# Kernel optimization log

Measured on AMD Instinct MI355X. Metric: run time of the kernel, lower is better.

## Reference

```python
import jax, jax.numpy as jnp
from jax import lax
import numpy as np

DIM = 384; NH = 8; N = 16; K = 4; DIN = 768; DTR = 24  # d_model, heads, d_state, d_conv, d_inner, dt_rank
B = 8; Hh = 48; Ww = 48


def _ln(x, g, b):
    m = jnp.mean(x, -1, keepdims=True)
    v = jnp.mean((x - m) ** 2, -1, keepdims=True)
    return (x - m) / jnp.sqrt(v + 1e-5) * g + b


def _mamba(x, in_w, in_b, conv_w, conv_b, xp_w, dt_w, dt_b, A_log, Dp, out_w, out_b):
    # x: (B, L, DIM)
    Bb, L, _ = x.shape
    xz = x @ in_w.T + in_b                      # (B, L, 2*DIN)
    xm, z = xz[..., :DIN], xz[..., DIN:]
    # depthwise causal conv over sequence
    xc = jnp.pad(xm.transpose(0, 2, 1), ((0, 0), (0, 0), (K - 1, 0)))  # (B, DIN, L+K-1)
    xconv = lax.conv_general_dilated(xc, conv_w[:, None, :], (1,), 'VALID',
                                     feature_group_count=DIN,
                                     dimension_numbers=('NCH', 'OIH', 'NCH'))
    u = jax.nn.silu((xconv + conv_b[None, :, None]).transpose(0, 2, 1))  # (B, L, DIN)
    dbc = u @ xp_w.T                            # (B, L, DTR + 2N)
    delta = jax.nn.softplus(dbc[..., :DTR] @ dt_w.T + dt_b)  # (B, L, DIN)
    Bm = dbc[..., DTR:DTR + N]                  # (B, L, N)
    Cm = dbc[..., DTR + N:]                     # (B, L, N)
    A = -jnp.exp(A_log)                         # (DIN, N)

    def step(h, inp):
        d_t, B_t, C_t, u_t = inp                # (B,DIN),(B,N),(B,N),(B,DIN)
        dA = jnp.exp(d_t[:, :, None] * A)       # (B, DIN, N)
        h = h * dA + d_t[:, :, None] * B_t[:, None, :] * u_t[:, :, None]
        y = jnp.einsum('bdn,bn->bd', h, C_t)
        return h, y

    h0 = jnp.zeros((Bb, DIN, N), x.dtype)
    xs = (delta.transpose(1, 0, 2), Bm.transpose(1, 0, 2), Cm.transpose(1, 0, 2), u.transpose(1, 0, 2))
    _, ys = lax.scan(step, h0, xs)
    y = ys.transpose(1, 0, 2) + u * Dp
    y = y * jax.nn.silu(z)
    return y @ out_w.T + out_b


def _forward(x, n1_g, n1_b, ap_w, ap_b, n2_g, n2_b, in_w, in_b, conv_w, conv_b, xp_w, dt_w, dt_b,
             A_log, Dp, out_w, out_b, mod_w1, mod_b1, mod_w2, mod_b2, n3_g, n3_b,
             fc1_w, fc1_b, fc2_w, fc2_b):
    Bb, C, Hc, Wc = x.shape
    xs = x.reshape(Bb, C, Hc * Wc).transpose(0, 2, 1)          # (B, L, C)
    xn = _ln(xs, n1_g, n1_b)
    attn = jax.nn.softmax(xn @ ap_w.T + ap_b, axis=1)          # softmax over sequence
    gc = jnp.einsum('bln,blc->bnc', attn, xn).mean(1)          # (B, C)
    mod = jax.nn.silu(gc @ mod_w1.T + mod_b1) @ mod_w2.T + mod_b2
    xn2 = _ln(xs, n2_g, n2_b)
    mo = _mamba(xn2, in_w, in_b, conv_w, conv_b, xp_w, dt_w, dt_b, A_log, Dp, out_w, out_b)
    mo = mo * (1.0 + mod[:, None, :])
    xs = xs + mo
    h = _ln(xs, n3_g, n3_b)
    h = jax.nn.gelu(h @ fc1_w.T + fc1_b) @ fc2_w.T + fc2_b
    xs = xs + h
    return xs.transpose(0, 2, 1).reshape(Bb, C, Hc, Wc)


def setup_inputs() -> dict:
    key = jax.random.key(0)
    ks = jax.random.split(key, 16)
    s = 0.02
    p = {}
    p['x'] = jax.random.normal(ks[0], (B, DIM, Hh, Ww), jnp.float32)
    p['n1_g'] = jnp.ones((DIM,), jnp.float32); p['n1_b'] = jnp.zeros((DIM,), jnp.float32)
    p['ap_w'] = jax.random.normal(ks[1], (NH, DIM), jnp.float32) * s; p['ap_b'] = jnp.zeros((NH,), jnp.float32)
    p['n2_g'] = jnp.ones((DIM,), jnp.float32); p['n2_b'] = jnp.zeros((DIM,), jnp.float32)
    p['in_w'] = jax.random.normal(ks[2], (2 * DIN, DIM), jnp.float32) * s; p['in_b'] = jnp.zeros((2 * DIN,), jnp.float32)
    p['conv_w'] = jax.random.normal(ks[3], (DIN, K), jnp.float32) * s; p['conv_b'] = jnp.zeros((DIN,), jnp.float32)
    p['xp_w'] = jax.random.normal(ks[4], (DTR + 2 * N, DIN), jnp.float32) * s
    p['dt_w'] = jax.random.normal(ks[5], (DIN, DTR), jnp.float32) * s
    p['dt_b'] = jax.random.uniform(ks[6], (DIN,), jnp.float32, minval=-4.0, maxval=-2.0)
    p['A_log'] = jnp.log(jnp.tile(jnp.arange(1, N + 1, dtype=jnp.float32), (DIN, 1)))
    p['Dp'] = jnp.ones((DIN,), jnp.float32)
    p['out_w'] = jax.random.normal(ks[7], (DIM, DIN), jnp.float32) * s; p['out_b'] = jnp.zeros((DIM,), jnp.float32)
    p['mod_w1'] = jax.random.normal(ks[8], (2 * DIM, DIM), jnp.float32) * s; p['mod_b1'] = jnp.zeros((2 * DIM,), jnp.float32)
    p['mod_w2'] = jax.random.normal(ks[9], (DIM, 2 * DIM), jnp.float32) * s; p['mod_b2'] = jnp.zeros((DIM,), jnp.float32)
    p['n3_g'] = jnp.ones((DIM,), jnp.float32); p['n3_b'] = jnp.zeros((DIM,), jnp.float32)
    p['fc1_w'] = jax.random.normal(ks[10], (4 * DIM, DIM), jnp.float32) * s; p['fc1_b'] = jnp.zeros((4 * DIM,), jnp.float32)
    p['fc2_w'] = jax.random.normal(ks[11], (DIM, 4 * DIM), jnp.float32) * s; p['fc2_b'] = jnp.zeros((DIM,), jnp.float32)
    return p


def reference(x, n1_g, n1_b, ap_w, ap_b, n2_g, n2_b, in_w, in_b, conv_w, conv_b, xp_w, dt_w, dt_b,
              A_log, Dp, out_w, out_b, mod_w1, mod_b1, mod_w2, mod_b2, n3_g, n3_b,
              fc1_w, fc1_b, fc2_w, fc2_b):
    return _forward(x, n1_g, n1_b, ap_w, ap_b, n2_g, n2_b, in_w, in_b, conv_w, conv_b, xp_w,
                    dt_w, dt_b, A_log, Dp, out_w, out_b, mod_w1, mod_b1, mod_w2, mod_b2,
                    n3_g, n3_b, fc1_w, fc1_b, fc2_w, fc2_b)
```

## Files before the change

kernel.cpp:

```cpp
#include <hip/hip_runtime.h>
#include <math.h>

#define DIMC 384
#define NHD 8
#define NSTATE 16
#define DINN 768
#define DTRK 24
#define BB 8
#define LSEQ 2304
#define MROWS (BB*LSEQ)
#define NCH 64
#define TCH 36
#define L2E 1.44269504f

typedef unsigned short u16;
typedef short bf16x8 __attribute__((ext_vector_type(8)));
typedef float f32x4 __attribute__((ext_vector_type(4)));

__device__ __forceinline__ float sigmoid_(float x){ return 1.f/(1.f+__expf(-x)); }
__device__ __forceinline__ float silu_(float x){ return x*sigmoid_(x); }
__device__ __forceinline__ float softplus_(float x){ return (x>20.f)?x:log1pf(__expf(x)); }
__device__ __forceinline__ float gelu_(float x){
  float x3=x*x*x;
  return 0.5f*x*(1.f+tanhf(0.7978845608028654f*(x+0.044715f*x3)));
}
__device__ __forceinline__ float bfu2f(u16 u){
  union{unsigned int i; float f;} c; c.i=((unsigned int)u)<<16; return c.f;
}
__device__ __forceinline__ u16 f2bfu(float f){
  union{float f; unsigned int i;} c; c.f=f;
  unsigned int r = c.i + 0x7FFFu + ((c.i>>16)&1u);
  return (u16)(r>>16);
}
__device__ __forceinline__ void gl_lds16(const u16* g, u16* l){
  __builtin_amdgcn_global_load_lds((__attribute__((address_space(1))) void*)g,
      (__attribute__((address_space(3))) void*)l, 16, 0, 0);
}

__device__ __forceinline__ u16 swzw(const float* __restrict__ s, int o, int KT,
                                    int Nsrc, int Ksrc){
  int e = o&7, l = (o>>3)&63, rest = o>>9;
  int kt = rest % KT, nt = rest / KT;
  int n = nt*16 + (l&15);
  int k = kt*32 + ((l>>4)<<3) + e;
  return (n<Nsrc && k<Ksrc) ? f2bfu(s[(size_t)n*Ksrc + k]) : (u16)0;
}

#define O1 589824
#define O2 688128
#define O3 983040
#define O4 1572864
#define O5 2162688
#define O6 2187264
#define OEND 2190336
__global__ void k_cvtall(const float* __restrict__ inw, const float* __restrict__ xpw,
    const float* __restrict__ outw, const float* __restrict__ fc1w,
    const float* __restrict__ fc2w, const float* __restrict__ dtw,
    u16* __restrict__ inw_b, u16* __restrict__ xpw_pad, u16* __restrict__ outw_b,
    u16* __restrict__ fc1w_b, u16* __restrict__ fc2w_b, u16* __restrict__ dtw_pad,
    float* __restrict__ gc){
  int i = blockIdx.x*256+threadIdx.x;
  if(i >= OEND) return;
  if(i < O1){ inw_b[i]   = swzw(inw,  i,    12, 1536, 384); }
  else if(i < O2){ xpw_pad[i-O1] = swzw(xpw,  i-O1, 24, 56,   768); }
  else if(i < O3){ outw_b[i-O2]  = swzw(outw, i-O2, 24, 384,  768); }
  else if(i < O4){ fc1w_b[i-O3]  = swzw(fc1w, i-O3, 12, 1536, 384); }
  else if(i < O5){ fc2w_b[i-O4]  = swzw(fc2w, i-O4, 48, 384,  1536); }
  else if(i < O6){ dtw_pad[i-O5] = swzw(dtw,  i-O5, 1,  768,  24); }
  else { gc[i-O6]=0.f; }
}

__global__ void k_transpose(const float* __restrict__ x, float* __restrict__ xs){
  __shared__ float tile[32][33];
  int b = blockIdx.z;
  int t0 = blockIdx.x*32, c0 = blockIdx.y*32;
  int tx = threadIdx.x, ty = threadIdx.y;
  const float* xb = x + (size_t)b*DIMC*LSEQ;
  #pragma unroll
  for(int q=0;q<4;q++)
    tile[ty+q*8][tx] = xb[(size_t)(c0+ty+q*8)*LSEQ + t0+tx];
  __syncthreads();
  float* xsb = xs + (size_t)b*LSEQ*DIMC;
  #pragma unroll
  for(int q=0;q<4;q++)
    xsb[(size_t)(t0+ty+q*8)*DIMC + c0+tx] = tile[tx][ty+q*8];
}

__global__ __launch_bounds__(64) void k_lnstats(const float* __restrict__ xs,
   const float* __restrict__ g1,const float* __restrict__ b1,
   const float* __restrict__ g2,const float* __restrict__ b2,
   const float* __restrict__ apw,const float* __restrict__ apb,
   float* __restrict__ meanr, float* __restrict__ rstdr,
   u16* __restrict__ xn2, float* __restrict__ scores){
  int row = blockIdx.x;
  int lane = threadIdx.x;
  const float* xr = xs + (size_t)row*DIMC;
  float v[6];
  float s=0.f, s2=0.f;
  #pragma unroll
  for(int i=0;i<6;i++){ v[i]=xr[lane+i*64]; s+=v[i]; s2+=v[i]*v[i]; }
  #pragma unroll
  for(int m=32;m>=1;m>>=1){ s += __shfl_xor(s,m); s2 += __shfl_xor(s2,m); }
  float mean = s*(1.f/DIMC);
  float var  = s2*(1.f/DIMC)-mean*mean;
  float rstd = rsqrtf(var+1e-5f);
  if(lane==0){ meanr[row]=mean; rstdr[row]=rstd; }
  float xv1[6];
  #pragma unroll
  for(int i=0;i<6;i++){
    int c = lane+i*64;
    float nx = (v[i]-mean)*rstd;
    xv1[i] = nx*g1[c]+b1[c];
    xn2[(size_t)row*DIMC+c] = f2bfu(nx*g2[c]+b2[c]);
  }
  #pragma unroll
  for(int h=0;h<NHD;h++){
    float p=0.f;
    #pragma unroll
    for(int i=0;i<6;i++) p += xv1[i]*apw[h*DIMC+lane+i*64];
    #pragma unroll
    for(int m=32;m>=1;m>>=1) p += __shfl_xor(p,m);
    if(lane==0) scores[(size_t)row*NHD+h]=p+apb[h];
  }
}

__global__ __launch_bounds__(256) void k_softmax_L(float* __restrict__ sc){
  int bh = blockIdx.x; int b = bh>>3, h = bh&7;
  int tid = threadIdx.x;
  __shared__ float red[8];
  const size_t base = (size_t)b*LSEQ*NHD + h;
  float mx = -1e30f;
  for(int l=tid;l<LSEQ;l+=256) mx = fmaxf(mx, sc[base + (size_t)l*NHD]);
  #pragma unroll
  for(int m=32;m>=1;m>>=1) mx = fmaxf(mx, __shfl_xor(mx,m));
  if((tid&63)==0) red[tid>>6]=mx;
  __syncthreads();
  mx = fmaxf(fmaxf(red[0],red[1]),fmaxf(red[2],red[3]));
  float sum=0.f;
  for(int l=tid;l<LSEQ;l+=256) sum += __expf(sc[base+(size_t)l*NHD]-mx);
  #pragma unroll
  for(int m=32;m>=1;m>>=1) sum += __shfl_xor(sum,m);
  if((tid&63)==0) red[4+(tid>>6)]=sum;
  __syncthreads();
  float inv = 1.f/(red[4]+red[5]+red[6]+red[7]);
  for(int l=tid;l<LSEQ;l+=256){
    size_t idx = base+(size_t)l*NHD;
    sc[idx] = __expf(sc[idx]-mx)*inv;
  }
}

__global__ __launch_bounds__(384) void k_gc(const float* __restrict__ attn,
    const float* __restrict__ xs, const float* __restrict__ meanr,
    const float* __restrict__ rstdr, const float* __restrict__ g1,
    const float* __restrict__ b1, float* __restrict__ gc){
  int b = blockIdx.x; int chunk = blockIdx.y; int c = threadIdx.x;
  int l0 = chunk*48;
  float acc=0.f, accw=0.f;
  for(int l=0;l<48;l++){
    int row = b*LSEQ + l0+l;
    const float* a = attn + (size_t)row*NHD;
    float ww = (((a[0]+a[1])+(a[2]+a[3]))+((a[4]+a[5])+(a[6]+a[7])))*0.125f;
    acc  += ww*(xs[(size_t)row*DIMC+c]-meanr[row])*rstdr[row];
    accw += ww;
  }
  atomicAdd(&gc[b*DIMC+c], acc*g1[c]+accw*b1[c]);
}

__global__ __launch_bounds__(256) void k_mod1(const float* __restrict__ gc,
    const float* __restrict__ w1, const float* __restrict__ b1,
    float* __restrict__ modh){
  int b = blockIdx.x; int n = blockIdx.y*64 + (threadIdx.x>>2);
  int sub = threadIdx.x&3;
  const float4* g = (const float4*)(gc + b*DIMC) + sub*24;
  const float4* wr = (const float4*)(w1 + (size_t)n*DIMC) + sub*24;
  float acc=0.f;
  #pragma unroll
  for(int k=0;k<24;k++){
    float4 a=g[k], w=wr[k];
    acc += a.x*w.x + a.y*w.y + a.z*w.z + a.w*w.w;
  }
  acc += __shfl_xor(acc,1); acc += __shfl_xor(acc,2);
  if(sub==0) modh[b*768+n] = silu_(acc+b1[n]);
}
__global__ __launch_bounds__(256) void k_mod2(const float* __restrict__ modh,
    const float* __restrict__ w2, const float* __restrict__ b2,
    float* __restrict__ mod){
  int b = blockIdx.x; int n = blockIdx.y*64 + (threadIdx.x>>2);
  int sub = threadIdx.x&3;
  const float4* g = (const float4*)(modh + b*768) + sub*48;
  const float4* wr = (const float4*)(w2 + (size_t)n*768) + sub*48;
  float acc=0.f;
  #pragma unroll
  for(int k=0;k<48;k++){
    float4 a=g[k], w=wr[k];
    acc += a.x*w.x + a.y*w.y + a.z*w.z + a.w*w.w;
  }
  acc += __shfl_xor(acc,1); acc += __shfl_xor(acc,2);
  if(sub==0) mod[b*DIMC+n] = acc+b2[n];
}

#define MG_STEP(KT_I, CUR, BIN, BOUT, VMSTR)                                   \
  {                                                                            \
    if((KT_I)+1 < KT){                                                         \
      _Pragma("unroll")                                                        \
      for(int j=0;j<4;j++)                                                     \
        BOUT[j] = *reinterpret_cast<const bf16x8*>(wp + 512 + j*(KT*512));     \
    }                                                                          \
    asm volatile("s_waitcnt " VMSTR ::: "memory");                             \
    __builtin_amdgcn_s_barrier();                                              \
    bf16x8 af[4];                                                              \
    {                                                                          \
      const u16* lbase = &lA[CUR][lofs];                                       \
      _Pragma("unroll")                                                        \
      for(int i=0;i<4;i++)                                                     \
        af[i] = *reinterpret_cast<const bf16x8*>(lbase + i*128);               \
    }                                                                          \
    asm volatile("s_waitcnt lgkmcnt(0)" ::: "memory");                         \
    __builtin_amdgcn_s_barrier();                                              \
    if((KT_I)+2 < KT){                                                         \
      gl_lds16(Ag0 + ((KT_I)+2)*32,      (CUR)? ld1 : ld0);                    \
      gl_lds16(Ag0 + ((KT_I)+2)*32 + 16, (CUR)? hd1 : hd0);                    \
    }                                                                          \
    _Pragma("unroll")                                                          \
    for(int i=0;i<4;i++)                                                       \
      _Pragma("unroll")                                                        \
      for(int j=0;j<4;j++)                                                     \
        acc[i][j] = __builtin_amdgcn_mfma_f32_16x16x32_bf16(af[i], BIN[j],     \
                                                            acc[i][j], 0,0,0);\
    wp += 512;                                                                 \
  }

template<int EPI, int K>
__global__ __launch_bounds__(256,4) void k_mgemm(
    const u16* __restrict__ A, const u16* __restrict__ Wf,
    const float* __restrict__ bias, void* __restrict__ outp,
    int N, const float* __restrict__ aux, void* __restrict__ outp2)
{
  constexpr int KT = K/32;
  __shared__ u16 lA[2][4096];
  int tid = threadIdx.x;
  int m0 = blockIdx.x*128, n0 = blockIdx.y*128;
  int wid = tid>>6, lane = tid&63;
  int wr = wid>>1, wc = wid&1;
  int lrow = lane&15, lk = lane>>4;
  f32x4 acc[4][4];
  #pragma unroll
  for(int i=0;i<4;i++)
    #pragma unroll
    for(int j=0;j<4;j++){ acc[i][j][0]=0.f; acc[i][j][1]=0.f; acc[i][j][2]=0.f; acc[i][j][3]=0.f; }

  int r0 = tid & 127, k0 = tid >> 7;
  const u16* Ag0 = A + (size_t)(m0+r0)*K + k0*8;
  const u16* wp  = Wf + ((size_t)((n0>>4) + wc*4)*KT)*512 + (size_t)lane*8;
  const int lofs = (lk*128 + wr*64 + lrow)*8;
  u16* ld0 = &lA[0][tid*8];  u16* hd0 = &lA[0][2048+tid*8];
  u16* ld1 = &lA[1][tid*8];  u16* hd1 = &lA[1][2048+tid*8];

  gl_lds16(Ag0,    ld0);
  gl_lds16(Ag0+16, hd0);
  if(KT>1){
    gl_lds16(Ag0+32, ld1);
    gl_lds16(Ag0+48, hd1);
  }
  bf16x8 bA[4], bB[4];
  #pragma unroll
  for(int j=0;j<4;j++) bA[j] = *reinterpret_cast<const bf16x8*>(wp + j*(KT*512));

  if(KT==1){
    MG_STEP(0, 0, bA, bB, "vmcnt(0)")
  } else {
    MG_STEP(0, 0, bA, bB, "vmcnt(4)")
    for(int kt=1; kt<KT-1; kt+=2){
      MG_STEP(kt,   1, bB, bA, "vmcnt(6)")
      MG_STEP(kt+1, 0, bA, bB, "vmcnt(6)")
    }
    MG_STEP(KT-1, 1, bB, bA, "vmcnt(0)")
  }

  #pragma unroll
  for(int i=0;i<4;i++){
    int row = m0 + wr*64 + i*16 + lk*4;
    #pragma unroll
    for(int j=0;j<4;j++){
      int col = n0 + wc*64 + j*16 + lrow;
      float bc = bias ? bias[col] : 0.f;
      f32x4 v = acc[i][j];
      if(EPI==0){
        u16* o = (u16*)outp;
        #pragma unroll
        for(int r=0;r<4;r++) o[(size_t)(row+r)*N + col] = f2bfu(v[r]+bc);
      } else if(EPI==1){
        u16* o = (u16*)outp;
        #pragma unroll
        for(int r=0;r<4;r++) o[(size_t)(row+r)*N + col] = f2bfu(gelu_(v[r]+bc));
      } else if(EPI==2){
        float* o = (float*)outp;
        int bi = row/LSEQ;
        float sc = 1.f + aux[bi*DIMC + col];
        #pragma unroll
        for(int r=0;r<4;r++) o[(size_t)(row+r)*DIMC + col] += (v[r]+bc)*sc;
      } else if(EPI==3){
        float* o = (float*)outp;
        int bi = row/LSEQ, t = row - bi*LSEQ;
        float4 s;
        s.x = aux[(size_t)(row+0)*DIMC+col] + v[0] + bc;
        s.y = aux[(size_t)(row+1)*DIMC+col] + v[1] + bc;
        s.z = aux[(size_t)(row+2)*DIMC+col] + v[2] + bc;
        s.w = aux[(size_t)(row+3)*DIMC+col] + v[3] + bc;
        *reinterpret_cast<float4*>(&o[((size_t)(bi*DIMC+col))*LSEQ + t]) = s;
      } else if(EPI==4){
        float* o = (float*)outp;
        if(col < N){
          #pragma unroll
          for(int r=0;r<4;r++) o[(size_t)(row+r)*N + col] = v[r]+bc;
        }
      } else if(EPI==5){
        u16* o = (col < 768) ? (u16*)outp : (u16*)outp2;
        int cc = (col < 768) ? col : col - 768;
        #pragma unroll
        for(int r=0;r<4;r++) o[(size_t)(row+r)*768 + cc] = f2bfu(v[r]+bc);
      } else if(EPI==6){
        float* o = (float*)outp;
        u16* o2 = (u16*)outp2;
        #pragma unroll
        for(int r=0;r<4;r++){
          float val = v[r];
          if(col < 56) o[(size_t)(row+r)*56 + col] = val;
          if(col < 32) o2[(size_t)(row+r)*32 + col] = (col<DTRK)? f2bfu(val) : (u16)0;
        }
      } else {
        u16* o = (u16*)outp;
        #pragma unroll
        for(int r=0;r<4;r++) o[(size_t)(row+r)*N + col] = f2bfu(softplus_(v[r]+bc));
      }
    }
  }
}

__global__ void k_conv(const u16* __restrict__ xm, const float* __restrict__ cw,
                       const float* __restrict__ cb, u16* __restrict__ u){
  int idx = blockIdx.x*256+threadIdx.x;
  if(idx >= MROWS*(DINN/8)) return;
  int j = idx % (DINN/8); int r = idx / (DINN/8);
  int t = r % LSEQ; int d0 = j*8;
  float4 w4_[8];
  #pragma unroll
  for(int e=0;e<8;e++) w4_[e] = reinterpret_cast<const float4*>(cw)[d0+e];
  float acc[8];
  #pragma unroll
  for(int e=0;e<8;e++) acc[e]=cb[d0+e];
  #pragma unroll
  for(int k=0;k<4;k++){
    int tt=t+k-3;
    if(tt>=0){
      uint4 v = *reinterpret_cast<const uint4*>(&xm[(size_t)(r+k-3)*DINN + d0]);
      unsigned vv[4]={v.x,v.y,v.z,v.w};
      #pragma unroll
      for(int e=0;e<8;e++){
        u16 raw = (e&1)? (u16)(vv[e>>1]>>16) : (u16)(vv[e>>1]&0xffffu);
        float wk = (k==0)? w4_[e].x : (k==1)? w4_[e].y : (k==2)? w4_[e].z : w4_[e].w;
        acc[e] += bfu2f(raw)*wk;
      }
    }
  }
  u16 outv[8];
  #pragma unroll
  for(int e=0;e<8;e++) outv[e]=f2bfu(silu_(acc[e]));
  *reinterpret_cast<uint4*>(&u[(size_t)r*DINN+d0]) = *reinterpret_cast<const uint4*>(outv);
}

__global__ __launch_bounds__(256) void k_scan1(
  const u16* __restrict__ dt_, const u16* __restrict__ u_,
  const float* __restrict__ dbc, const float* __restrict__ alog,
  float* __restrict__ ssum, float* __restrict__ hloc)
{
  __shared__ float Bsh[TCH][16];
  int bid = blockIdx.x;
  int b = bid/(NCH*3); int rem = bid%(NCH*3); int ch = rem/3; int dblk = rem%3;
  int tid = threadIdx.x; int d = dblk*256 + tid;
  size_t rbase = (size_t)b*LSEQ + (size_t)ch*TCH;
  for(int j=tid; j<TCH*16; j+=256){
    int row=j>>4, n=j&15;
    Bsh[row][n] = dbc[(rbase+row)*56 + DTRK + n];
  }
  float Acl2[16];
  float a0 = -__expf(alog[(size_t)d*16])*L2E;
  bool fast = true;
  #pragma unroll
  for(int n=0;n<16;n++){
    Acl2[n] = -__expf(alog[(size_t)d*16+n])*L2E;
    float tgt = (float)(n+1)*a0;
    fast = fast && (fabsf(Acl2[n]-tgt) <= 1e-4f*fabsf(tgt));
  }
  float h[16];
  #pragma unroll
  for(int n=0;n<16;n++) h[n]=0.f;
  float S=0.f;
  const u16* dtp = dt_ + rbase*DINN + d;
  const u16* up  = u_  + rbase*DINN + d;
  __syncthreads();
  if(fast){
    for(int t=0;t<TCH;t++){
      float dt = bfu2f(dtp[(size_t)t*DINN]);
      float uv = bfu2f(up[(size_t)t*DINN]);
      float G = dt*uv;
      S += dt;
      float e = exp2f(dt*a0), w = e;
      const float4* b4 = (const float4*)Bsh[t];
      float4 B0=b4[0],B1=b4[1],B2=b4[2],B3=b4[3];
      float Bv[16]={B0.x,B0.y,B0.z,B0.w,B1.x,B1.y,B1.z,B1.w,
                    B2.x,B2.y,B2.z,B2.w,B3.x,B3.y,B3.z,B3.w};
      #pragma unroll
      for(int n=0;n<16;n++){ h[n] = h[n]*w + G*Bv[n]; w *= e; }
    }
  } else {
    for(int t=0;t<TCH;t++){
      float dt = bfu2f(dtp[(size_t)t*DINN]);
      float uv = bfu2f(up[(size_t)t*DINN]);
      float G = dt*uv;
      S += dt;
      const float4* b4 = (const float4*)Bsh[t];
      float4 B0=b4[0],B1=b4[1],B2=b4[2],B3=b4[3];
      float Bv[16]={B0.x,B0.y,B0.z,B0.w,B1.x,B1.y,B1.z,B1.w,
                    B2.x,B2.y,B2.z,B2.w,B3.x,B3.y,B3.z,B3.w};
      #pragma unroll
      for(int n=0;n<16;n++) h[n] = h[n]*exp2f(dt*Acl2[n]) + G*Bv[n];
    }
  }
  ssum[((size_t)b*NCH+ch)*DINN + d] = S;
  float* hp = hloc + (((size_t)b*NCH+ch)*DINN + d)*16;
  #pragma unroll
  for(int n=0;n<16;n++) hp[n] = h[n];
}

__global__ __launch_bounds__(256) void k_scan2(
  const float* __restrict__ ssum, const float* __restrict__ alog,
  float* __restrict__ hl)
{
  int gid = blockIdx.x*256+threadIdx.x;
  int n = gid & 15; int d = (gid>>4)%DINN; int b = gid/(DINN*NSTATE);
  float Acl2 = -__expf(alog[(size_t)d*16+n])*L2E;
  float hin=0.f;
  for(int ch=0; ch<NCH; ch++){
    size_t sidx = ((size_t)b*NCH+ch)*DINN + d;
    size_t idx  = sidx*16 + n;
    float a = exp2f(ssum[sidx]*Acl2);
    float hold = hl[idx];
    hl[idx] = hin;
    hin = a*hin + hold;
  }
}

__global__ __launch_bounds__(256) void k_scan3(
  const u16* __restrict__ dt_, u16* uy, const u16* __restrict__ z_,
  const float* __restrict__ dbc, const float* __restrict__ alog,
  const float* __restrict__ Dp, const float* __restrict__ hin)
{
  __shared__ float BC[TCH][32];
  int bid = blockIdx.x;
  int b = bid/(NCH*3); int rem = bid%(NCH*3); int ch = rem/3; int dblk = rem%3;
  int tid = threadIdx.x; int d = dblk*256 + tid;
  size_t rbase = (size_t)b*LSEQ + (size_t)ch*TCH;
  for(int j=tid; j<TCH*32; j+=256){
    int row=j>>5, c=j&31;
    BC[row][c] = dbc[(rbase+row)*56 + DTRK + c];
  }
  float Acl2[16], h[16];
  const float* hp = hin + (((size_t)b*NCH+ch)*DINN + d)*16;
  float a0 = -__expf(alog[(size_t)d*16])*L2E;
  bool fast = true;
  #pragma unroll
  for(int n=0;n<16;n++){
    Acl2[n] = -__expf(alog[(size_t)d*16+n])*L2E;
    float tgt = (float)(n+1)*a0;
    fast = fast && (fabsf(Acl2[n]-tgt) <= 1e-4f*fabsf(tgt));
    h[n] = hp[n];
  }
  float Dv = Dp[d];
  const u16* dtp = dt_ + rbase*DINN + d;
  u16*       uyp = uy  + rbase*DINN + d;
  const u16* zp  = z_  + rbase*DINN + d;
  __syncthreads();
  if(fast){
    for(int t=0;t<TCH;t++){
      float dt = bfu2f(dtp[(size_t)t*DINN]);
      float uv = bfu2f(uyp[(size_t)t*DINN]);
      float zv = bfu2f(zp[(size_t)t*DINN]);
      float G = dt*uv;
      float e = exp2f(dt*a0), w = e;
      const float4* bc4 = (const float4*)BC[t];
      float4 B0=bc4[0],B1=bc4[1],B2=bc4[2],B3=bc4[3];
      float4 C0=bc4[4],C1=bc4[5],C2=bc4[6],C3=bc4[7];
      float Bv[16]={B0.x,B0.y,B0.z,B0.w,B1.x,B1.y,B1.z,B1.w,
                    B2.x,B2.y,B2.z,B2.w,B3.x,B3.y,B3.z,B3.w};
      float Cv[16]={C0.x,C0.y,C0.z,C0.w,C1.x,C1.y,C1.z,C1.w,
                    C2.x,C2.y,C2.z,C2.w,C3.x,C3.y,C3.z,C3.w};
      float y0=0.f,y1=0.f,y2=0.f,y3=0.f;
      #pragma unroll
      for(int n=0;n<16;n++){
        h[n] = h[n]*w + G*Bv[n];
        w *= e;
        if((n&3)==0) y0 += h[n]*Cv[n];
        else if((n&3)==1) y1 += h[n]*Cv[n];
        else if((n&3)==2) y2 += h[n]*Cv[n];
        else y3 += h[n]*Cv[n];
      }
      float y = (y0+y1)+(y2+y3);
      uyp[(size_t)t*DINN] = f2bfu((y + uv*Dv)*silu_(zv));
    }
  } else {
    for(int t=0;t<TCH;t++){
      float dt = bfu2f(dtp[(size_t)t*DINN]);
      float uv = bfu2f(uyp[(size_t)t*DINN]);
      float zv = bfu2f(zp[(size_t)t*DINN]);
      float G = dt*uv;
      const float4* bc4 = (const float4*)BC[t];
      float4 B0=bc4[0],B1=bc4[1],B2=bc4[2],B3=bc4[3];
      float4 C0=bc4[4],C1=bc4[5],C2=bc4[6],C3=bc4[7];
      float Bv[16]={B0.x,B0.y,B0.z,B0.w,B1.x,B1.y,B1.z,B1.w,
                    B2.x,B2.y,B2.z,B2.w,B3.x,B3.y,B3.z,B3.w};
      float Cv[16]={C0.x,C0.y,C0.z,C0.w,C1.x,C1.y,C1.z,C1.w,
                    C2.x,C2.y,C2.z,C2.w,C3.x,C3.y,C3.z,C3.w};
      float y0=0.f,y1=0.f,y2=0.f,y3=0.f;
      #pragma unroll
      for(int n=0;n<16;n++){
        h[n] = h[n]*exp2f(dt*Acl2[n]) + G*Bv[n];
        if((n&3)==0) y0 += h[n]*Cv[n];
        else if((n&3)==1) y1 += h[n]*Cv[n];
        else if((n&3)==2) y2 += h[n]*Cv[n];
        else y3 += h[n]*Cv[n];
      }
      float y = (y0+y1)+(y2+y3);
      uyp[(size_t)t*DINN] = f2bfu((y + uv*Dv)*silu_(zv));
    }
  }
}

__global__ __launch_bounds__(64) void k_ln3(const float* __restrict__ xin,
    const float* __restrict__ g, const float* __restrict__ bb, u16* __restrict__ xout){
  int row = blockIdx.x;
  int lane = threadIdx.x;
  const float* xr = xin + (size_t)row*DIMC;
  float v[6];
  float s=0.f, s2=0.f;
  #pragma unroll
  for(int i=0;i<6;i++){ v[i]=xr[lane+i*64]; s+=v[i]; s2+=v[i]*v[i]; }
  #pragma unroll
  for(int m=32;m>=1;m>>=1){ s += __shfl_xor(s,m); s2 += __shfl_xor(s2,m); }
  float mean = s*(1.f/DIMC);
  float var  = s2*(1.f/DIMC)-mean*mean;
  float rstd = rsqrtf(var+1e-5f);
  #pragma unroll
  for(int i=0;i<6;i++){
    int c = lane+i*64;
    xout[(size_t)row*DIMC+c] = f2bfu((v[i]-mean)*rstd*g[c]+bb[c]);
  }
}

extern "C" void kernel_launch(void* const* d_in, const int* in_sizes, int n_in,
                              void* d_out, int out_size, void* d_ws, size_t ws_size,
                              hipStream_t stream)
{
  const float* x     = (const float*)d_in[0];
  const float* n1g   = (const float*)d_in[1];
  const float* n1b   = (const float*)d_in[2];
  const float* apw   = (const float*)d_in[3];
  const float* apb   = (const float*)d_in[4];
  const float* n2g   = (const float*)d_in[5];
  const float* n2b   = (const float*)d_in[6];
  const float* inw   = (const float*)d_in[7];
  const float* inb   = (const float*)d_in[8];
  const float* convw = (const float*)d_in[9];
  const float* convb = (const float*)d_in[10];
  const float* xpw   = (const float*)d_in[11];
  const float* dtw   = (const float*)d_in[12];
  const float* dtb   = (const float*)d_in[13];
  const float* Alog  = (const float*)d_in[14];
  const float* Dp    = (const float*)d_in[15];
  const float* outw  = (const float*)d_in[16];
  const float* outb  = (const float*)d_in[17];
  const float* modw1 = (const float*)d_in[18];
  const float* modb1 = (const float*)d_in[19];
  const float* modw2 = (const float*)d_in[20];
  const float* modb2 = (const float*)d_in[21];
  const float* n3g   = (const float*)d_in[22];
  const float* n3b   = (const float*)d_in[23];
  const float* fc1w  = (const float*)d_in[24];
  const float* fc1b  = (const float*)d_in[25];
  const float* fc2w  = (const float*)d_in[26];
  const float* fc2b  = (const float*)d_in[27];

  float* ws = (float*)d_ws;
  float* XS    = ws;
  float* R1    = ws + 7077888;
  u16*   XMb   = (u16*)R1;
  u16*   DTb   = (u16*)R1;
  float* SSUM  = R1 + 7077888;
  float* HL    = R1 + 7471104;
  u16*   F1b   = (u16*)R1;
  u16*   Zb    = (u16*)(ws + 21233664);
  float* DBC   = ws + 28311552;
  float* WB    = ws + 29343744;
  u16*   inw_b   = (u16*)WB;
  u16*   xpw_pad = inw_b + 589824;
  u16*   outw_b  = xpw_pad + 98304;
  u16*   fc1w_b  = outw_b + 294912;
  u16*   fc2w_b  = fc1w_b + 589824;
  float* SCORES= ws + 30425088;
  float* MEANR = ws + 30590976;
  float* RSTDR = ws + 30609408;
  float* GC    = ws + 30627840;
  float* MODH  = ws + 30630912;
  float* MOD   = ws + 30637056;
  u16*   DT32b = (u16*)(ws + 30640128);
  u16*   dtw_pad=(u16*)(ws + 30935040);
  (void)ws_size; (void)n_in; (void)in_sizes; (void)out_size;

  u16* XN2b = (u16*)d_out;
  u16* Ub   = (u16*)d_out;
  u16* Hb   = (u16*)d_out;

  k_cvtall<<<(OEND+255)/256, 256, 0, stream>>>(inw, xpw, outw, fc1w, fc2w, dtw,
      inw_b, xpw_pad, outw_b, fc1w_b, fc2w_b, dtw_pad, GC);

  k_transpose<<<dim3(72,12,8), dim3(32,8), 0, stream>>>(x, XS);
  k_lnstats<<<MROWS, 64, 0, stream>>>(XS, n1g,n1b,n2g,n2b, apw,apb, MEANR, RSTDR, XN2b, SCORES);
  k_softmax_L<<<BB*NHD, 256, 0, stream>>>(SCORES);
  k_gc<<<dim3(BB,48), 384, 0, stream>>>(SCORES, XS, MEANR, RSTDR, n1g, n1b, GC);
  k_mod1<<<dim3(BB,12), 256, 0, stream>>>(GC, modw1, modb1, MODH);
  k_mod2<<<dim3(BB,6), 256, 0, stream>>>(MODH, modw2, modb2, MOD);

  k_mgemm<5,384><<<dim3(144,12), 256, 0, stream>>>(XN2b, inw_b, inb, XMb, 1536, nullptr, Zb);
  k_conv<<<(MROWS*(DINN/8)+255)/256, 256, 0, stream>>>(XMb, convw, convb, Ub);
  k_mgemm<6,768><<<dim3(144,1), 256, 0, stream>>>(Ub, xpw_pad, nullptr, DBC, 56, nullptr, DT32b);
  k_mgemm<7,32><<<dim3(144,6), 256, 0, stream>>>(DT32b, dtw_pad, dtb, DTb, 768, nullptr, nullptr);
  k_scan1<<<BB*NCH*3, 256, 0, stream>>>(DTb, Ub, DBC, Alog, SSUM, HL);
  k_scan2<<<384, 256, 0, stream>>>(SSUM, Alog, HL);
  k_scan3<<<BB*NCH*3, 256, 0, stream>>>(DTb, Ub, Zb, DBC, Alog, Dp, HL);
  k_mgemm<2,768><<<dim3(144,3), 256, 0, stream>>>(Ub, outw_b, outb, XS, 384, MOD, nullptr);
  k_ln3<<<MROWS, 64, 0, stream>>>(XS, n3g, n3b, Hb);
  k_mgemm<1,384><<<dim3(144,12), 256, 0, stream>>>(Hb, fc1w_b, fc1b, F1b, 1536, nullptr, nullptr);
  k_mgemm<3,1536><<<dim3(144,3), 256, 0, stream>>>(F1b, fc2w_b, fc2b, d_out, 384, XS, nullptr);
}
```

Measured before the change: 490.1 us.

## Triple-buffer GEMM LDS pipeline and split-K the x_proj GEMM

The bf16 MFMA GEMM moves from a two-stage LDS double buffer with two barriers per k-step to a three-stage ring with one barrier per step. The next A tile is issued right after that barrier, before the current tile is read. Launch bounds rise to 6 blocks per SM. The x_proj GEMM, which launched only 144 blocks, is split four ways over K through blockIdx.z, writing fp32 partials that a new reduction kernel sums into DBC and the padded dt input. This is meant to hide more load latency and fill the GPU better, at the cost of extra LDS per block, a partial-sum buffer and one more kernel launch.

After: 1.794 ms. 3.66x slower.

```diff
diff --git a/kernel.cpp b/kernel.cpp
--- a/kernel.cpp
+++ b/kernel.cpp
@@ -199,84 +199,11 @@
   if(sub==0) mod[b*DIMC+n] = acc+b2[n];
 }
 
-#define MG_STEP(KT_I, CUR, BIN, BOUT, VMSTR)                                   \
-  {                                                                            \
-    if((KT_I)+1 < KT){                                                         \
-      _Pragma("unroll")                                                        \
-      for(int j=0;j<4;j++)                                                     \
-        BOUT[j] = *reinterpret_cast<const bf16x8*>(wp + 512 + j*(KT*512));     \
-    }                                                                          \
-    asm volatile("s_waitcnt " VMSTR ::: "memory");                             \
-    __builtin_amdgcn_s_barrier();                                              \
-    bf16x8 af[4];                                                              \
-    {                                                                          \
-      const u16* lbase = &lA[CUR][lofs];                                       \
-      _Pragma("unroll")                                                        \
-      for(int i=0;i<4;i++)                                                     \
-        af[i] = *reinterpret_cast<const bf16x8*>(lbase + i*128);               \
-    }                                                                          \
-    asm volatile("s_waitcnt lgkmcnt(0)" ::: "memory");                         \
-    __builtin_amdgcn_s_barrier();                                              \
-    if((KT_I)+2 < KT){                                                         \
-      gl_lds16(Ag0 + ((KT_I)+2)*32,      (CUR)? ld1 : ld0);                    \
-      gl_lds16(Ag0 + ((KT_I)+2)*32 + 16, (CUR)? hd1 : hd0);                    \
-    }                                                                          \
-    _Pragma("unroll")                                                          \
-    for(int i=0;i<4;i++)                                                       \
-      _Pragma("unroll")                                                        \
-      for(int j=0;j<4;j++)                                                     \
-        acc[i][j] = __builtin_amdgcn_mfma_f32_16x16x32_bf16(af[i], BIN[j],     \
-                                                            acc[i][j], 0,0,0);\
-    wp += 512;                                                                 \
-  }
-
-template<int EPI, int K>
-__global__ __launch_bounds__(256,4) void k_mgemm(
-    const u16* __restrict__ A, const u16* __restrict__ Wf,
-    const float* __restrict__ bias, void* __restrict__ outp,
-    int N, const float* __restrict__ aux, void* __restrict__ outp2)
+template<int EPI>
+__device__ __forceinline__ void mg_epilogue(
+    f32x4 (&acc)[4][4], int m0, int n0, int wr, int wc, int lrow, int lk,
+    const float* bias, void* outp, int N, const float* aux, void* outp2)
 {
-  constexpr int KT = K/32;
-  __shared__ u16 lA[2][4096];
-  int tid = threadIdx.x;
-  int m0 = blockIdx.x*128, n0 = blockIdx.y*128;
-  int wid = tid>>6, lane = tid&63;
-  int wr = wid>>1, wc = wid&1;
-  int lrow = lane&15, lk = lane>>4;
-  f32x4 acc[4][4];
-  #pragma unroll
-  for(int i=0;i<4;i++)
-    #pragma unroll
-    for(int j=0;j<4;j++){ acc[i][j][0]=0.f; acc[i][j][1]=0.f; acc[i][j][2]=0.f; acc[i][j][3]=0.f; }
-
-  int r0 = tid & 127, k0 = tid >> 7;
-  const u16* Ag0 = A + (size_t)(m0+r0)*K + k0*8;
-  const u16* wp  = Wf + ((size_t)((n0>>4) + wc*4)*KT)*512 + (size_t)lane*8;
-  const int lofs = (lk*128 + wr*64 + lrow)*8;
-  u16* ld0 = &lA[0][tid*8];  u16* hd0 = &lA[0][2048+tid*8];
-  u16* ld1 = &lA[1][tid*8];  u16* hd1 = &lA[1][2048+tid*8];
-
-  gl_lds16(Ag0,    ld0);
-  gl_lds16(Ag0+16, hd0);
-  if(KT>1){
-    gl_lds16(Ag0+32, ld1);
-    gl_lds16(Ag0+48, hd1);
-  }
-  bf16x8 bA[4], bB[4];
-  #pragma unroll
-  for(int j=0;j<4;j++) bA[j] = *reinterpret_cast<const bf16x8*>(wp + j*(KT*512));
-
-  if(KT==1){
-    MG_STEP(0, 0, bA, bB, "vmcnt(0)")
-  } else {
-    MG_STEP(0, 0, bA, bB, "vmcnt(4)")
-    for(int kt=1; kt<KT-1; kt+=2){
-      MG_STEP(kt,   1, bB, bA, "vmcnt(6)")
-      MG_STEP(kt+1, 0, bA, bB, "vmcnt(6)")
-    }
-    MG_STEP(KT-1, 1, bB, bA, "vmcnt(0)")
-  }
-
   #pragma unroll
   for(int i=0;i<4;i++){
     int row = m0 + wr*64 + i*16 + lk*4;
@@ -319,15 +246,6 @@
         int cc = (col < 768) ? col : col - 768;
         #pragma unroll
         for(int r=0;r<4;r++) o[(size_t)(row+r)*768 + cc] = f2bfu(v[r]+bc);
-      } else if(EPI==6){
-        float* o = (float*)outp;
-        u16* o2 = (u16*)outp2;
-        #pragma unroll
-        for(int r=0;r<4;r++){
-          float val = v[r];
-          if(col < 56) o[(size_t)(row+r)*56 + col] = val;
-          if(col < 32) o2[(size_t)(row+r)*32 + col] = (col<DTRK)? f2bfu(val) : (u16)0;
-        }
       } else {
         u16* o = (u16*)outp;
         #pragma unroll
@@ -335,6 +253,113 @@
       }
     }
   }
+}
+
+#define MG_STEP3(KT_I, CUR, STG, BIN, BOUT, VMSTR)                             \
+  {                                                                            \
+    if((KT_I)+1 < KT){                                                         \
+      _Pragma("unroll")                                                        \
+      for(int j=0;j<4;j++)                                                     \
+        BOUT[j] = *reinterpret_cast<const bf16x8*>(wp + 512 + j*(KTTOT*512));  \
+    }                                                                          \
+    asm volatile("s_waitcnt " VMSTR ::: "memory");                             \
+    __builtin_amdgcn_s_barrier();                                              \
+    if((KT_I)+2 < KT){                                                         \
+      gl_lds16(Ag0 + ((KT_I)+2)*32,      &lA[STG][tid*8]);                     \
+      gl_lds16(Ag0 + ((KT_I)+2)*32 + 16, &lA[STG][2048+tid*8]);                \
+    }                                                                          \
+    bf16x8 af[4];                                                              \
+    {                                                                          \
+      const u16* lbase = &lA[CUR][lofs];                                       \
+      _Pragma("unroll")                                                        \
+      for(int i=0;i<4;i++)                                                     \
+        af[i] = *reinterpret_cast<const bf16x8*>(lbase + i*128);               \
+    }                                                                          \
+    asm volatile("s_waitcnt lgkmcnt(0)" ::: "memory");                         \
+    __builtin_amdgcn_sched_barrier(0);                                         \
+    _Pragma("unroll")                                                          \
+    for(int i=0;i<4;i++)                                                       \
+      _Pragma("unroll")                                                        \
+      for(int j=0;j<4;j++)                                                     \
+        acc[i][j] = __builtin_amdgcn_mfma_f32_16x16x32_bf16(af[i], BIN[j],     \
+                                                            acc[i][j], 0,0,0);\
+    wp += 512;                                                                 \
+  }
+
+template<int EPI, int KLOOP, int KSTRIDE = KLOOP>
+__global__ __launch_bounds__(256,6) void k_mgemm(
+    const u16* __restrict__ A, const u16* __restrict__ Wf,
+    const float* __restrict__ bias, void* __restrict__ outp,
+    int N, const float* __restrict__ aux, void* __restrict__ outp2)
+{
+  constexpr int KT = KLOOP/32;
+  constexpr int KTTOT = KSTRIDE/32;
+  __shared__ u16 lA[3][4096];
+  int tid = threadIdx.x;
+  int m0 = blockIdx.x*128, n0 = blockIdx.y*128;
+  int wid = tid>>6, lane = tid&63;
+  int wr = wid>>1, wc = wid&1;
+  int lrow = lane&15, lk = lane>>4;
+  f32x4 acc[4][4];
+  #pragma unroll
+  for(int i=0;i<4;i++)
+    #pragma unroll
+    for(int j=0;j<4;j++){ acc[i][j][0]=0.f; acc[i][j][1]=0.f; acc[i][j][2]=0.f; acc[i][j][3]=0.f; }
+
+  int r0 = tid & 127, k0 = tid >> 7;
+  size_t zofsA = 0, zofsW = 0;
+  if(KSTRIDE != KLOOP){
+    zofsA = (size_t)blockIdx.z * KLOOP;
+    zofsW = (size_t)blockIdx.z * KT * 512;
+    outp  = (float*)outp + (size_t)blockIdx.z * MROWS * N;
+  }
+  const u16* Ag0 = A + (size_t)(m0+r0)*KSTRIDE + zofsA + k0*8;
+  const u16* wp  = Wf + ((size_t)((n0>>4) + wc*4)*KTTOT)*512 + zofsW + (size_t)lane*8;
+  const int lofs = (lk*128 + wr*64 + lrow)*8;
+
+  gl_lds16(Ag0,    &lA[0][tid*8]);
+  gl_lds16(Ag0+16, &lA[0][2048+tid*8]);
+  if(KT>1){
+    gl_lds16(Ag0+32, &lA[1][tid*8]);
+    gl_lds16(Ag0+48, &lA[1][2048+tid*8]);
+  }
+  bf16x8 bA[4], bB[4];
+  #pragma unroll
+  for(int j=0;j<4;j++) bA[j] = *reinterpret_cast<const bf16x8*>(wp + j*(KTTOT*512));
+
+  if(KT==1){
+    MG_STEP3(0, 0, 0, bA, bB, "vmcnt(0)")
+  } else {
+    int kt=0;
+    for(; kt+6<KT; kt+=6){
+      MG_STEP3(kt+0, 0, 2, bA, bB, "vmcnt(6)")
+      MG_STEP3(kt+1, 1, 0, bB, bA, "vmcnt(6)")
+      MG_STEP3(kt+2, 2, 1, bA, bB, "vmcnt(6)")
+      MG_STEP3(kt+3, 0, 2, bB, bA, "vmcnt(6)")
+      MG_STEP3(kt+4, 1, 0, bA, bB, "vmcnt(6)")
+      MG_STEP3(kt+5, 2, 1, bB, bA, "vmcnt(6)")
+    }
+    MG_STEP3(kt+0, 0, 2, bA, bB, "vmcnt(6)")
+    MG_STEP3(kt+1, 1, 0, bB, bA, "vmcnt(6)")
+    MG_STEP3(kt+2, 2, 1, bA, bB, "vmcnt(6)")
+    MG_STEP3(kt+3, 0, 2, bB, bA, "vmcnt(6)")
+    MG_STEP3(kt+4, 1, 0, bA, bB, "vmcnt(6)")
+    MG_STEP3(kt+5, 2, 1, bB, bA, "vmcnt(0)")
+  }
+
+  mg_epilogue<EPI>(acc, m0, n0, wr, wc, lrow, lk, bias, outp, N, aux, outp2);
+}
+
+__global__ void k_xpred(const float* __restrict__ P, float* __restrict__ dbc,
+                        u16* __restrict__ dt32){
+  int idx = blockIdx.x*256+threadIdx.x;
+  if(idx >= MROWS*56) return;
+  int row = idx/56, c = idx - row*56;
+  float s = P[idx] + P[idx + (size_t)MROWS*56] + P[idx + (size_t)2*MROWS*56]
+          + P[idx + (size_t)3*MROWS*56];
+  dbc[idx] = s;
+  if(c < DTRK) dt32[(size_t)row*32 + c] = f2bfu(s);
+  if(c < 8)    dt32[(size_t)row*32 + DTRK + c] = 0;
 }
 
 __global__ void k_conv(const u16* __restrict__ xm, const float* __restrict__ cw,
@@ -597,6 +622,7 @@
   u16*   DTb   = (u16*)R1;
   float* SSUM  = R1 + 7077888;
   float* HL    = R1 + 7471104;
+  float* XPP   = HL;
   u16*   F1b   = (u16*)R1;
   u16*   Zb    = (u16*)(ws + 21233664);
   float* DBC   = ws + 28311552;
@@ -632,7 +658,8 @@
 
   k_mgemm<5,384><<<dim3(144,12), 256, 0, stream>>>(XN2b, inw_b, inb, XMb, 1536, nullptr, Zb);
   k_conv<<<(MROWS*(DINN/8)+255)/256, 256, 0, stream>>>(XMb, convw, convb, Ub);
-  k_mgemm<6,768><<<dim3(144,1), 256, 0, stream>>>(Ub, xpw_pad, nullptr, DBC, 56, nullptr, DT32b);
+  k_mgemm<4,192,768><<<dim3(144,1,4), 256, 0, stream>>>(Ub, xpw_pad, nullptr, XPP, 56, nullptr, nullptr);
+  k_xpred<<<(MROWS*56+255)/256, 256, 0, stream>>>(XPP, DBC, DT32b);
   k_mgemm<7,32><<<dim3(144,6), 256, 0, stream>>>(DT32b, dtw_pad, dtb, DTb, 768, nullptr, nullptr);
   k_scan1<<<BB*NCH*3, 256, 0, stream>>>(DTb, Ub, DBC, Alog, SSUM, HL);
   k_scan2<<<384, 256, 0, stream>>>(SSUM, Alog, HL);
```
